# Optimization experiments

Measured on AMD Instinct MI355X. Metric: run time of the kernel, lower is better.

Reference implementation:

```python
import jax, jax.numpy as jnp
import numpy as np

B, S, E = 2, 4096, 768
NH, D = 12, 64
W = 256            # one-sided attention window (attention_window=512 // 2)
NEG = jnp.float32(-1e30)  # stands in for -inf at invalid band positions (safe grads)


def setup_inputs() -> dict:
    key = jax.random.key(0)
    ks = jax.random.split(key, 4)
    sc = 0.02
    return {
        'hidden_states': jax.random.normal(ks[0], (B, S, E), jnp.float32),
        'attention_mask': jnp.zeros((B, S), jnp.float32),   # 0 = local attention everywhere
        'is_index_masked': jnp.zeros((B, S), bool),
        'Wq': jax.random.normal(ks[1], (E, E), jnp.float32) * sc,
        'bq': jnp.zeros((E,), jnp.float32),
        'Wk': jax.random.normal(ks[2], (E, E), jnp.float32) * sc,
        'bk': jnp.zeros((E,), jnp.float32),
        'Wv': jax.random.normal(ks[3], (E, E), jnp.float32) * sc,
        'bv': jnp.zeros((E,), jnp.float32),
    }


def _longformer_local(hidden_states, attention_mask, is_index_masked, Wq, bq, Wk, bk, Wv, bv):
    b, s, e = hidden_states.shape
    w = W
    nc = s // w
    # projections (nn.Linear: x @ W.T + b); query pre-scaled by 1/sqrt(head_dim)
    q = (hidden_states @ Wq.T + bq) / jnp.sqrt(jnp.float32(D))
    k = hidden_states @ Wk.T + bk
    v = hidden_states @ Wv.T + bv
    # [B, NH, S, D]
    q = q.reshape(b, s, NH, D).transpose(0, 2, 1, 3)
    k = k.reshape(b, s, NH, D).transpose(0, 2, 1, 3)
    v = v.reshape(b, s, NH, D).transpose(0, 2, 1, 3)

    # pad keys/values by w on each side; chunk into [B,NH,nc,3w,D] windows
    kp = jnp.pad(k, ((0, 0), (0, 0), (w, w), (0, 0)))
    vp = jnp.pad(v, ((0, 0), (0, 0), (w, w), (0, 0)))
    starts = jnp.arange(nc) * w                      # [nc]
    cidx = starts[:, None] + jnp.arange(3 * w)[None, :]  # [nc, 3w] (padded coords)
    kc = kp[:, :, cidx, :]                            # [B,NH,nc,3w,D]
    vc = vp[:, :, cidx, :]                            # [B,NH,nc,3w,D]
    qc = q.reshape(b, NH, nc, w, D)

    # banded scores: query p in chunk attends keys at offsets p..p+2w within the 3w window
    scores = jnp.einsum('bhcpd,bhckd->bhcpk', qc, kc)  # [B,NH,nc,w,3w]
    p = jnp.arange(w)[:, None]
    koff = jnp.arange(2 * w + 1)[None, :]
    band_idx = p + koff                                # [w, 2w+1]
    band = jnp.take_along_axis(scores, band_idx[None, None, None], axis=-1)  # [B,NH,nc,w,2w+1]

    # additive mask from attention_mask (torch: finfo.min where !=0), gathered at key positions
    fmask = jnp.where(attention_mask != 0, jnp.finfo(jnp.float32).min, jnp.float32(0.0))  # [B,S]
    j = starts[:, None, None] + band_idx[None] - w     # global key index [nc,w,2w+1]
    valid = (j >= 0) & (j < s)
    jc = jnp.clip(j, 0, s - 1)
    band = band + fmask[:, jc][:, None]                # [B,1->NH,nc,w,2w+1]
    # _mask_invalid_locations: out-of-sequence band entries -> -inf (NEG)
    band = jnp.where(valid[None, None], band, NEG)

    probs = jax.nn.softmax(band.astype(jnp.float32), axis=-1)
    # zero probs at fully-masked query positions
    im = is_index_masked.reshape(b, 1, nc, w, 1)
    probs = jnp.where(im, jnp.float32(0.0), probs)

    # scatter band back to [B,NH,nc,w,3w] and contract with value chunks
    full = jnp.zeros((b, NH, nc, w, 3 * w), probs.dtype).at[:, :, :, p, band_idx].set(probs)
    out = jnp.einsum('bhcpk,bhckd->bhcpd', full, vc)   # [B,NH,nc,w,D]
    out = out.reshape(b, NH, s, D).transpose(0, 2, 1, 3).reshape(b, s, e)
    return out


def reference(hidden_states, attention_mask, is_index_masked, Wq, bq, Wk, bk, Wv, bv):
    return _longformer_local(hidden_states, attention_mask, is_index_masked,
                             Wq, bq, Wk, bk, Wv, bv)
```

## Files before the change

kernel.cpp:

```cpp
#include <hip/hip_runtime.h>

typedef __bf16 bf16;
typedef __attribute__((ext_vector_type(8))) __bf16 bf16x8;
typedef __attribute__((ext_vector_type(4))) __bf16 bf16x4;
typedef __attribute__((ext_vector_type(4))) float f32x4;

#define MFMA16(a, b, c) __builtin_amdgcn_mfma_f32_16x16x32_bf16((a), (b), (c), 0, 0, 0)

#define S_LEN 4096
#define NHEAD 12
#define EMB   768
#define NEGV  (-1e30f)

__device__ __forceinline__ void gload16(const bf16* g, bf16* l) {
  __builtin_amdgcn_global_load_lds((const __attribute__((address_space(1))) void*)g,
                                   (__attribute__((address_space(3))) void*)l, 16, 0, 0);
}

__global__ __launch_bounds__(256) void cvt_kernel(const float* __restrict__ x,
                                                  bf16* __restrict__ o, int n8, float scale) {
  int i = blockIdx.x * 256 + threadIdx.x;
  if (i >= n8) return;
  const float4* p = (const float4*)(x + (size_t)i * 8);
  float4 a = p[0], b = p[1];
  bf16x8 v;
  v[0] = (bf16)(a.x * scale); v[1] = (bf16)(a.y * scale);
  v[2] = (bf16)(a.z * scale); v[3] = (bf16)(a.w * scale);
  v[4] = (bf16)(b.x * scale); v[5] = (bf16)(b.y * scale);
  v[6] = (bf16)(b.z * scale); v[7] = (bf16)(b.w * scale);
  *(bf16x8*)(o + (size_t)i * 8) = v;
}

__global__ __launch_bounds__(256) void cvt3_kernel(const float* __restrict__ w0,
                                                   const float* __restrict__ w1,
                                                   const float* __restrict__ w2,
                                                   bf16* __restrict__ o, int n8) {
  int which = blockIdx.y;
  const float* src = (which == 0) ? w0 : (which == 1) ? w1 : w2;
  float scale = (which == 0) ? 0.125f : 1.0f;
  int i = blockIdx.x * 256 + threadIdx.x;
  if (i >= n8) return;
  const float4* p = (const float4*)(src + (size_t)i * 8);
  float4 a = p[0], b = p[1];
  bf16x8 v;
  v[0] = (bf16)(a.x * scale); v[1] = (bf16)(a.y * scale);
  v[2] = (bf16)(a.z * scale); v[3] = (bf16)(a.w * scale);
  v[4] = (bf16)(b.x * scale); v[5] = (bf16)(b.y * scale);
  v[6] = (bf16)(b.z * scale); v[7] = (bf16)(b.w * scale);
  *(bf16x8*)(o + ((size_t)which * n8 + i) * 8) = v;
}

__global__ __launch_bounds__(256) void amask_cvt(const float* __restrict__ am,
                                                 float* __restrict__ o, int n) {
  int i = blockIdx.x * 256 + threadIdx.x;
  if (i < n) o[i] = (am[i] != 0.f) ? -1e30f : 0.f;
}

__global__ __launch_bounds__(256) void qkv_gemm(const bf16* __restrict__ Xb, const bf16* __restrict__ Wb,
                                                const float* __restrict__ bq, const float* __restrict__ bk,
                                                const float* __restrict__ bv,
                                                bf16* __restrict__ Qo, bf16* __restrict__ Ko,
                                                bf16* __restrict__ Vt) {
  __shared__ union SM {
    struct { bf16 a[2][128 * 64]; bf16 b2[2][128 * 64]; } st;
    bf16 c[128 * 130];
  } sm;
  const int tid = threadIdx.x;
  const int l = tid & 63, w = tid >> 6;
  const int ln = l & 15, g = l >> 4;
  const int wm = w >> 1, wn = w & 1;
  const int m0 = blockIdx.x * 128;
  const int n0 = blockIdx.y * 128;

  const f32x4 zero4 = {0.f, 0.f, 0.f, 0.f};
  f32x4 acc[4][4];
#pragma unroll
  for (int i = 0; i < 4; ++i)
#pragma unroll
    for (int j = 0; j < 4; ++j) acc[i][j] = zero4;

  int srow[4], sslot[4];
#pragma unroll
  for (int i = 0; i < 4; ++i) {
    const int G = w * 256 + i * 64 + l;
    srow[i] = G >> 3;
    sslot[i] = (G & 7) ^ (srow[i] & 7);
  }

  auto stage = [&](int sb, int kt) {
    const int k0 = kt * 64;
#pragma unroll
    for (int i = 0; i < 4; ++i) {
      gload16(Xb + (size_t)(m0 + srow[i]) * 768 + k0 + sslot[i] * 8, &sm.st.a[sb][(w * 256 + i * 64) * 8]);
      gload16(Wb + (size_t)(n0 + srow[i]) * 768 + k0 + sslot[i] * 8, &sm.st.b2[sb][(w * 256 + i * 64) * 8]);
    }
  };

  stage(0, 0);
  __syncthreads();

  int buf = 0;
  for (int kt = 0; kt < 12; ++kt, buf ^= 1) {
    if (kt < 11) stage(buf ^ 1, kt + 1);
#pragma unroll
    for (int kc = 0; kc < 2; ++kc) {
      bf16x8 af[4], bfr[4];
#pragma unroll
      for (int i = 0; i < 4; ++i) {
        int ra = wm * 64 + i * 16 + ln;
        af[i] = *(const bf16x8*)(&sm.st.a[buf][ra * 64 + ((kc * 4 + g) ^ (ra & 7)) * 8]);
        int rb = wn * 64 + i * 16 + ln;
        bfr[i] = *(const bf16x8*)(&sm.st.b2[buf][rb * 64 + ((kc * 4 + g) ^ (rb & 7)) * 8]);
      }
#pragma unroll
      for (int mi = 0; mi < 4; ++mi)
#pragma unroll
        for (int ni = 0; ni < 4; ++ni)
          acc[mi][ni] = MFMA16(af[mi], bfr[ni], acc[mi][ni]);
    }
    __syncthreads();
  }

  const int which = n0 / 768;
  const int h0 = (n0 % 768) >> 6;
  const int b = m0 >> 12;
  const int h = h0 + wn;
  const float bsc = (which == 0) ? 0.125f : 1.0f;
  const float* bias = (which == 0) ? bq : (which == 1) ? bk : bv;
  float bvv[4];
#pragma unroll
  for (int ni = 0; ni < 4; ++ni) bvv[ni] = bias[h * 64 + ni * 16 + ln] * bsc;

#pragma unroll
  for (int mi = 0; mi < 4; ++mi)
#pragma unroll
    for (int ni = 0; ni < 4; ++ni)
#pragma unroll
      for (int r = 0; r < 4; ++r) {
        int sl = wm * 64 + mi * 16 + g * 4 + r;
        sm.c[sl * 130 + wn * 64 + ni * 16 + ln] = (bf16)(acc[mi][ni][r] + bvv[ni]);
      }
  __syncthreads();

  if (which < 2) {
    bf16* dst = (which == 0) ? Qo : Ko;
#pragma unroll
    for (int it = 0; it < 8; ++it) {
      int gid = it * 256 + tid;
      int sl = gid >> 4, cg = gid & 15;
      int hh = h0 + (cg >> 3);
      bf16x8 v8 = *(const bf16x8*)(&sm.c[sl * 130 + cg * 8]);
      *(bf16x8*)(dst + ((size_t)(b * NHEAD + hh) * S_LEN + (m0 & 4095) + sl) * 64 + (cg & 7) * 8) = v8;
    }
  } else {
#pragma unroll
    for (int it = 0; it < 4; ++it) {
      int d = it * 32 + (tid >> 3);
      int scp = tid & 7;
      int hh = h0 + (d >> 6);
      bf16x8 o0, o1;
#pragma unroll
      for (int i2 = 0; i2 < 8; ++i2) o0[i2] = sm.c[(scp * 16 + i2) * 130 + d];
#pragma unroll
      for (int i2 = 0; i2 < 8; ++i2) o1[i2] = sm.c[(scp * 16 + 8 + i2) * 130 + d];
      bf16* dp = Vt + ((size_t)(b * NHEAD + hh) * 64 + (d & 63)) * S_LEN + (m0 & 4095) + scp * 16;
      *(bf16x8*)dp = o0;
      *(bf16x8*)(dp + 8) = o1;
    }
  }
}

__global__ __launch_bounds__(512) void attn_kernel(const bf16* __restrict__ Qb, const bf16* __restrict__ Kb,
                                                   const bf16* __restrict__ Vtb,
                                                   const float* __restrict__ Amadd,
                                                   const unsigned char* __restrict__ imask,
                                                   float* __restrict__ out) {
  __shared__ bf16 Ks[2][64 * 64];
  __shared__ bf16 Vs[2][64 * 64];
  __shared__ bf16 Pt[8][16 * 64];
  const int tid = threadIdx.x;
  const int l = tid & 63, w = tid >> 6;
  const int ln = l & 15, g = l >> 4;
  const int orig = blockIdx.x;
  const int lb = (orig & 7) * 96 + (orig >> 3);
  const int qc = lb & 31, bh = lb >> 5;
  const int b = bh / NHEAD, h = bh % NHEAD;
  const int q0 = qc * 128;
  const int qg = q0 + w * 16 + ln;

  const size_t qoff = ((size_t)bh * S_LEN + qg) * 64;
  const bf16x8 qf0 = *(const bf16x8*)(Qb + qoff + g * 8);
  const bf16x8 qf1 = *(const bf16x8*)(Qb + qoff + 32 + g * 8);
  const float* Ab = Amadd + b * S_LEN;

  const f32x4 zero4 = {0.f, 0.f, 0.f, 0.f};
  f32x4 acc[4];
#pragma unroll
  for (int i = 0; i < 4; ++i) acc[i] = zero4;
  float mrun = -1e38f, lrun = 0.f;

  const int t_lo = (q0 >= 256) ? 0 : ((256 - q0) >> 6);
  int t_hi = (S_LEN + 256 - q0) >> 6;
  if (t_hi > 10) t_hi = 10;

  auto stage = [&](int sb, int t) {
    const int tj0 = q0 - 256 + t * 64;
    const int G = w * 64 + l;
    const int row = G >> 3, dsl = G & 7;
    const int slot = dsl ^ (row & 7);
    gload16(Kb + ((size_t)bh * S_LEN + tj0 + row) * 64 + slot * 8, &Ks[sb][w * 512]);
    gload16(Vtb + ((size_t)bh * 64 + row) * S_LEN + tj0 + slot * 8, &Vs[sb][w * 512]);
  };

  stage(0, t_lo);
  asm volatile("s_waitcnt vmcnt(0)" ::: "memory");
  __syncthreads();

  int buf = 0;
  for (int t = t_lo; t < t_hi; ++t, buf ^= 1) {
    const int tj0 = q0 - 256 + t * 64;

    f32x4 am[4];
#pragma unroll
    for (int mi = 0; mi < 4; ++mi) am[mi] = *(const f32x4*)(Ab + tj0 + mi * 16 + g * 4);

    if (t + 1 < t_hi) stage(buf ^ 1, t + 1);

    f32x4 sc[4];
#pragma unroll
    for (int i = 0; i < 4; ++i) sc[i] = zero4;
    __builtin_amdgcn_s_setprio(1);
#pragma unroll
    for (int kc = 0; kc < 2; ++kc) {
      bf16x8 qf = kc ? qf1 : qf0;
#pragma unroll
      for (int mi = 0; mi < 4; ++mi) {
        int r = mi * 16 + ln;
        bf16x8 kf = *(const bf16x8*)(&Ks[buf][r * 64 + ((kc * 4 + g) ^ (r & 7)) * 8]);
        sc[mi] = MFMA16(kf, qf, sc[mi]);
      }
    }
    __builtin_amdgcn_s_setprio(0);

    float mt = -1e38f;
    const bool full = (t * 64 >= w * 16 + 15) && (t * 64 <= w * 16 + 449);
    if (full) {
#pragma unroll
      for (int mi = 0; mi < 4; ++mi)
#pragma unroll
        for (int r = 0; r < 4; ++r) {
          float v = sc[mi][r] + am[mi][r];
          sc[mi][r] = v;
          mt = fmaxf(mt, v);
        }
    } else {
#pragma unroll
      for (int mi = 0; mi < 4; ++mi)
#pragma unroll
        for (int r = 0; r < 4; ++r) {
          int j = tj0 + mi * 16 + g * 4 + r;
          bool valid = (j >= qg - 256) && (j <= qg + 256);
          float v = valid ? (sc[mi][r] + am[mi][r]) : NEGV;
          sc[mi][r] = v;
          mt = fmaxf(mt, v);
        }
    }
    mt = fmaxf(mt, __shfl_xor(mt, 16));
    mt = fmaxf(mt, __shfl_xor(mt, 32));
    if (!__all(mt <= mrun + 8.f)) {
      float mnew = fmaxf(mrun, mt);
      float corr = __expf(mrun - mnew);
      lrun *= corr;
#pragma unroll
      for (int i = 0; i < 4; ++i) acc[i] *= corr;
      mrun = mnew;
    }
    float psum = 0.f;
    float pv[4][4];
#pragma unroll
    for (int mi = 0; mi < 4; ++mi)
#pragma unroll
      for (int r = 0; r < 4; ++r) {
        float p = __expf(sc[mi][r] - mrun);
        pv[mi][r] = p;
        psum += p;
      }
    psum += __shfl_xor(psum, 16);
    psum += __shfl_xor(psum, 32);
    lrun += psum;

    bf16* PtW = &Pt[w][0];
#pragma unroll
    for (int mi = 0; mi < 4; ++mi) {
      bf16x4 pk;
      pk[0] = (bf16)pv[mi][0]; pk[1] = (bf16)pv[mi][1];
      pk[2] = (bf16)pv[mi][2]; pk[3] = (bf16)pv[mi][3];
      *(bf16x4*)(&PtW[ln * 64 + ((mi * 4 + g) ^ ln) * 4]) = pk;
    }

    __builtin_amdgcn_s_setprio(1);
#pragma unroll
    for (int ds2 = 0; ds2 < 4; ++ds2) {
#pragma unroll
      for (int kc = 0; kc < 2; ++kc) {
        int r = ds2 * 16 + ln;
        bf16x8 vf = *(const bf16x8*)(&Vs[buf][r * 64 + ((kc * 4 + g) ^ (r & 7)) * 8]);
        bf16x4 pa = *(const bf16x4*)(&PtW[ln * 64 + ((kc * 8 + g * 2) ^ ln) * 4]);
        bf16x4 pb = *(const bf16x4*)(&PtW[ln * 64 + ((kc * 8 + g * 2 + 1) ^ ln) * 4]);
        bf16x8 pf = __builtin_shufflevector(pa, pb, 0, 1, 2, 3, 4, 5, 6, 7);
        acc[ds2] = MFMA16(vf, pf, acc[ds2]);
      }
    }
    __builtin_amdgcn_s_setprio(0);

    asm volatile("s_waitcnt vmcnt(0)" ::: "memory");
    __builtin_amdgcn_s_barrier();
    __builtin_amdgcn_sched_barrier(0);
  }

  float rl = 1.0f / lrun;
  if (imask[b * S_LEN + qg] != 0) rl = 0.0f;
  float* ob = out + ((size_t)b * S_LEN + qg) * EMB + h * 64;
#pragma unroll
  for (int ds2 = 0; ds2 < 4; ++ds2) {
    float4 o;
    o.x = acc[ds2][0] * rl; o.y = acc[ds2][1] * rl;
    o.z = acc[ds2][2] * rl; o.w = acc[ds2][3] * rl;
    *(float4*)(ob + ds2 * 16 + g * 4) = o;
  }
}

extern "C" void kernel_launch(void* const* d_in, const int* in_sizes, int n_in,
                              void* d_out, int out_size, void* d_ws, size_t ws_size,
                              hipStream_t stream) {
  const float* X = (const float*)d_in[0];
  const float* amask = (const float*)d_in[1];
  const unsigned char* imask = (const unsigned char*)d_in[2];
  const float* Wq = (const float*)d_in[3];
  const float* bq = (const float*)d_in[4];
  const float* Wk = (const float*)d_in[5];
  const float* bk = (const float*)d_in[6];
  const float* Wv = (const float*)d_in[7];
  const float* bv = (const float*)d_in[8];
  float* out = (float*)d_out;

  bf16* Xb = (bf16*)d_ws;
  bf16* Wb = Xb + 6291456;
  bf16* Qb = Wb + 3 * 589824;
  bf16* Kb = Qb + 6291456;
  bf16* Vt = Kb + 6291456;
  float* Amadd = (float*)(Vt + 6291456);

  cvt_kernel<<<3072, 256, 0, stream>>>(X, Xb, 6291456 / 8, 1.0f);
  cvt3_kernel<<<dim3(288, 3), 256, 0, stream>>>(Wq, Wk, Wv, Wb, 589824 / 8);
  amask_cvt<<<32, 256, 0, stream>>>(amask, Amadd, 2 * S_LEN);
  qkv_gemm<<<dim3(64, 18), 256, 0, stream>>>(Xb, Wb, bq, bk, bv, Qb, Kb, Vt);
  attn_kernel<<<768, 512, 0, stream>>>(Qb, Kb, Vt, Amadd, imask, out);
}
```

Baseline: 177.1 us.

## Shrink attention blocks, pass probabilities via lane shuffles, fuse mask conversion

The attention kernel now runs 256-thread blocks covering 64 queries, launched as 1536 blocks with a launch-bounds occupancy hint. Each block walks 9 key tiles instead of 10, which cuts the redundant edge-tile work that the wider 128-query window needed. The P matrix no longer goes through shared memory: probabilities are transposed in registers with cross-lane shuffles, which removes the LDS writes, reads and the Pt buffer. The attention mask is stored as bf16 and its conversion is folded into the weight-conversion launch, saving one kernel launch at the cost of more K/V reloads per query across the smaller blocks.

```diff
diff --git a/kernel.cpp b/kernel.cpp
--- a/kernel.cpp
+++ b/kernel.cpp
@@ -4,6 +4,8 @@
 typedef __attribute__((ext_vector_type(8))) __bf16 bf16x8;
 typedef __attribute__((ext_vector_type(4))) __bf16 bf16x4;
 typedef __attribute__((ext_vector_type(4))) float f32x4;
+typedef __attribute__((ext_vector_type(2))) unsigned int u32x2;
+typedef __attribute__((ext_vector_type(4))) int i32x4;
 
 #define MFMA16(a, b, c) __builtin_amdgcn_mfma_f32_16x16x32_bf16((a), (b), (c), 0, 0, 0)
 
@@ -34,8 +36,15 @@
 __global__ __launch_bounds__(256) void cvt3_kernel(const float* __restrict__ w0,
                                                    const float* __restrict__ w1,
                                                    const float* __restrict__ w2,
-                                                   bf16* __restrict__ o, int n8) {
+                                                   bf16* __restrict__ o, int n8,
+                                                   const float* __restrict__ amask,
+                                                   bf16* __restrict__ am_out) {
   int which = blockIdx.y;
+  if (which == 3) {
+    int i = blockIdx.x * 256 + threadIdx.x;
+    if (i < 2 * S_LEN) am_out[i] = (amask[i] != 0.f) ? (bf16)(-1e30f) : (bf16)0.f;
+    return;
+  }
   const float* src = (which == 0) ? w0 : (which == 1) ? w1 : w2;
   float scale = (which == 0) ? 0.125f : 1.0f;
   int i = blockIdx.x * 256 + threadIdx.x;
@@ -48,12 +57,6 @@
   v[4] = (bf16)(b.x * scale); v[5] = (bf16)(b.y * scale);
   v[6] = (bf16)(b.z * scale); v[7] = (bf16)(b.w * scale);
   *(bf16x8*)(o + ((size_t)which * n8 + i) * 8) = v;
-}
-
-__global__ __launch_bounds__(256) void amask_cvt(const float* __restrict__ am,
-                                                 float* __restrict__ o, int n) {
-  int i = blockIdx.x * 256 + threadIdx.x;
-  if (i < n) o[i] = (am[i] != 0.f) ? -1e30f : 0.f;
 }
 
 __global__ __launch_bounds__(256) void qkv_gemm(const bf16* __restrict__ Xb, const bf16* __restrict__ Wb,
@@ -170,28 +173,27 @@
   }
 }
 
-__global__ __launch_bounds__(512) void attn_kernel(const bf16* __restrict__ Qb, const bf16* __restrict__ Kb,
-                                                   const bf16* __restrict__ Vtb,
-                                                   const float* __restrict__ Amadd,
-                                                   const unsigned char* __restrict__ imask,
-                                                   float* __restrict__ out) {
+__global__ __launch_bounds__(256, 5) void attn_kernel(const bf16* __restrict__ Qb, const bf16* __restrict__ Kb,
+                                                      const bf16* __restrict__ Vtb,
+                                                      const bf16* __restrict__ Amb,
+                                                      const unsigned char* __restrict__ imask,
+                                                      float* __restrict__ out) {
   __shared__ bf16 Ks[2][64 * 64];
   __shared__ bf16 Vs[2][64 * 64];
-  __shared__ bf16 Pt[8][16 * 64];
   const int tid = threadIdx.x;
   const int l = tid & 63, w = tid >> 6;
   const int ln = l & 15, g = l >> 4;
   const int orig = blockIdx.x;
-  const int lb = (orig & 7) * 96 + (orig >> 3);
-  const int qc = lb & 31, bh = lb >> 5;
+  const int lb = (orig & 7) * 192 + (orig >> 3);
+  const int qc = lb & 63, bh = lb >> 6;
   const int b = bh / NHEAD, h = bh % NHEAD;
-  const int q0 = qc * 128;
+  const int q0 = qc * 64;
   const int qg = q0 + w * 16 + ln;
 
   const size_t qoff = ((size_t)bh * S_LEN + qg) * 64;
   const bf16x8 qf0 = *(const bf16x8*)(Qb + qoff + g * 8);
   const bf16x8 qf1 = *(const bf16x8*)(Qb + qoff + 32 + g * 8);
-  const float* Ab = Amadd + b * S_LEN;
+  const bf16* Ab = Amb + b * S_LEN;
 
   const f32x4 zero4 = {0.f, 0.f, 0.f, 0.f};
   f32x4 acc[4];
@@ -201,28 +203,33 @@
 
   const int t_lo = (q0 >= 256) ? 0 : ((256 - q0) >> 6);
   int t_hi = (S_LEN + 256 - q0) >> 6;
-  if (t_hi > 10) t_hi = 10;
+  if (t_hi > 9) t_hi = 9;
 
   auto stage = [&](int sb, int t) {
     const int tj0 = q0 - 256 + t * 64;
-    const int G = w * 64 + l;
-    const int row = G >> 3, dsl = G & 7;
-    const int slot = dsl ^ (row & 7);
-    gload16(Kb + ((size_t)bh * S_LEN + tj0 + row) * 64 + slot * 8, &Ks[sb][w * 512]);
-    gload16(Vtb + ((size_t)bh * 64 + row) * S_LEN + tj0 + slot * 8, &Vs[sb][w * 512]);
+#pragma unroll
+    for (int p = 0; p < 2; ++p) {
+      const int G = p * 256 + w * 64 + l;
+      const int row = G >> 3, dsl = G & 7;
+      const int slot = dsl ^ (row & 7);
+      gload16(Kb + ((size_t)bh * S_LEN + tj0 + row) * 64 + slot * 8, &Ks[sb][(p * 256 + w * 64) * 8]);
+      gload16(Vtb + ((size_t)bh * 64 + row) * S_LEN + tj0 + slot * 8, &Vs[sb][(p * 256 + w * 64) * 8]);
+    }
   };
 
   stage(0, t_lo);
   asm volatile("s_waitcnt vmcnt(0)" ::: "memory");
   __syncthreads();
 
+  const bool b5 = (l & 32) != 0, b4 = (l & 16) != 0;
+
   int buf = 0;
   for (int t = t_lo; t < t_hi; ++t, buf ^= 1) {
     const int tj0 = q0 - 256 + t * 64;
 
-    f32x4 am[4];
-#pragma unroll
-    for (int mi = 0; mi < 4; ++mi) am[mi] = *(const f32x4*)(Ab + tj0 + mi * 16 + g * 4);
+    bf16x4 am4[4];
+#pragma unroll
+    for (int mi = 0; mi < 4; ++mi) am4[mi] = *(const bf16x4*)(Ab + tj0 + mi * 16 + g * 4);
 
     if (t + 1 < t_hi) stage(buf ^ 1, t + 1);
 
@@ -249,7 +256,7 @@
       for (int mi = 0; mi < 4; ++mi)
 #pragma unroll
         for (int r = 0; r < 4; ++r) {
-          float v = sc[mi][r] + am[mi][r];
+          float v = sc[mi][r] + (float)am4[mi][r];
           sc[mi][r] = v;
           mt = fmaxf(mt, v);
         }
@@ -260,7 +267,7 @@
         for (int r = 0; r < 4; ++r) {
           int j = tj0 + mi * 16 + g * 4 + r;
           bool valid = (j >= qg - 256) && (j <= qg + 256);
-          float v = valid ? (sc[mi][r] + am[mi][r]) : NEGV;
+          float v = valid ? (sc[mi][r] + (float)am4[mi][r]) : NEGV;
           sc[mi][r] = v;
           mt = fmaxf(mt, v);
         }
@@ -276,26 +283,37 @@
       mrun = mnew;
     }
     float psum = 0.f;
-    float pv[4][4];
-#pragma unroll
-    for (int mi = 0; mi < 4; ++mi)
-#pragma unroll
-      for (int r = 0; r < 4; ++r) {
-        float p = __expf(sc[mi][r] - mrun);
-        pv[mi][r] = p;
-        psum += p;
-      }
+    u32x2 pku[4];
+#pragma unroll
+    for (int mi = 0; mi < 4; ++mi) {
+      float p0 = __expf(sc[mi][0] - mrun), p1 = __expf(sc[mi][1] - mrun);
+      float p2 = __expf(sc[mi][2] - mrun), p3 = __expf(sc[mi][3] - mrun);
+      psum += (p0 + p1) + (p2 + p3);
+      bf16x4 pk;
+      pk[0] = (bf16)p0; pk[1] = (bf16)p1; pk[2] = (bf16)p2; pk[3] = (bf16)p3;
+      pku[mi] = __builtin_bit_cast(u32x2, pk);
+    }
     psum += __shfl_xor(psum, 16);
     psum += __shfl_xor(psum, 32);
     lrun += psum;
 
-    bf16* PtW = &Pt[w][0];
-#pragma unroll
-    for (int mi = 0; mi < 4; ++mi) {
-      bf16x4 pk;
-      pk[0] = (bf16)pv[mi][0]; pk[1] = (bf16)pv[mi][1];
-      pk[2] = (bf16)pv[mi][2]; pk[3] = (bf16)pv[mi][3];
-      *(bf16x4*)(&PtW[ln * 64 + ((mi * 4 + g) ^ ln) * 4]) = pk;
+    bf16x8 pf[2];
+#pragma unroll
+    for (int kc = 0; kc < 2; ++kc) {
+      u32x2 R0 = pku[2 * kc], R1 = pku[2 * kc + 1];
+      u32x2 s, e;
+      s = b5 ? R0 : R1;
+      e[0] = (unsigned)__shfl_xor((int)s[0], 32);
+      e[1] = (unsigned)__shfl_xor((int)s[1], 32);
+      R0 = b5 ? e : R0;
+      R1 = b5 ? R1 : e;
+      s = b4 ? R0 : R1;
+      e[0] = (unsigned)__shfl_xor((int)s[0], 16);
+      e[1] = (unsigned)__shfl_xor((int)s[1], 16);
+      R0 = b4 ? e : R0;
+      R1 = b4 ? R1 : e;
+      i32x4 q4 = {(int)R0[0], (int)R0[1], (int)R1[0], (int)R1[1]};
+      pf[kc] = __builtin_bit_cast(bf16x8, q4);
     }
 
     __builtin_amdgcn_s_setprio(1);
@@ -305,10 +323,7 @@
       for (int kc = 0; kc < 2; ++kc) {
         int r = ds2 * 16 + ln;
         bf16x8 vf = *(const bf16x8*)(&Vs[buf][r * 64 + ((kc * 4 + g) ^ (r & 7)) * 8]);
-        bf16x4 pa = *(const bf16x4*)(&PtW[ln * 64 + ((kc * 8 + g * 2) ^ ln) * 4]);
-        bf16x4 pb = *(const bf16x4*)(&PtW[ln * 64 + ((kc * 8 + g * 2 + 1) ^ ln) * 4]);
-        bf16x8 pf = __builtin_shufflevector(pa, pb, 0, 1, 2, 3, 4, 5, 6, 7);
-        acc[ds2] = MFMA16(vf, pf, acc[ds2]);
+        acc[ds2] = MFMA16(vf, pf[kc], acc[ds2]);
       }
     }
     __builtin_amdgcn_s_setprio(0);
@@ -349,11 +364,10 @@
   bf16* Qb = Wb + 3 * 589824;
   bf16* Kb = Qb + 6291456;
   bf16* Vt = Kb + 6291456;
-  float* Amadd = (float*)(Vt + 6291456);
+  bf16* Amb = Vt + 6291456;
 
   cvt_kernel<<<3072, 256, 0, stream>>>(X, Xb, 6291456 / 8, 1.0f);
-  cvt3_kernel<<<dim3(288, 3), 256, 0, stream>>>(Wq, Wk, Wv, Wb, 589824 / 8);
-  amask_cvt<<<32, 256, 0, stream>>>(amask, Amadd, 2 * S_LEN);
+  cvt3_kernel<<<dim3(288, 4), 256, 0, stream>>>(Wq, Wk, Wv, Wb, 589824 / 8, amask, Amb);
   qkv_gemm<<<dim3(64, 18), 256, 0, stream>>>(Xb, Wb, bq, bk, bv, Qb, Kb, Vt);
-  attn_kernel<<<768, 512, 0, stream>>>(Qb, Kb, Vt, Amadd, imask, out);
-}
+  attn_kernel<<<1536, 256, 0, stream>>>(Qb, Kb, Vt, Amb, imask, out);
+}
```

Result: no change. 177.4 us (+0.1%).
